# Kernel optimization log

Hardware: AMD Instinct MI355X
Metric: run time of the kernel (lower is better)

## Reference

```python
import jax, jax.numpy as jnp
import numpy as np


def setup_inputs() -> dict:
    key = jax.random.key(0)
    k1, k2, k3, k4 = jax.random.split(key, 4)
    B, C, H, W = 4, 48, 512, 512
    T, ws = 3, 64
    # factor matrices (per TensorMultiplication_einsum, T summation terms)
    # init scale: 1/(init_temperature**(1/3) * sqrt(out_dim)) with init_temperature=1.0
    Ws = jax.random.normal(k2, (T, ws, ws), jnp.float32) / np.sqrt(ws)
    Hs = jax.random.normal(k3, (T, ws, ws), jnp.float32) / np.sqrt(ws)
    Cs = jax.random.normal(k4, (T, C, C), jnp.float32) / np.sqrt(C)
    x = jax.random.normal(k1, (B, C, H, W), jnp.float32)
    return {"x": x, "Ws": Ws, "Hs": Hs, "Cs": Cs, "window_size": ws}


def reference(x, Ws, Hs, Cs, window_size):
    """FeatureProcessingBlock forward:
      window_partition -> sum_t einsum('bchw,wW,hH,cC->bCHW') -> window_reverse.
    The window partition/reverse reshapes are fused into one einsum over the
    blocked view (p,q index the window grid; h,w index within-window pixels).
    """
    B, C, H, W = x.shape
    ws = window_size
    # (B, C, H//ws, ws, W//ws, ws)
    xb = x.reshape(B, C, H // ws, ws, W // ws, ws)
    # sum over T terms and contract w, h, c axes with their factor matrices
    out = jnp.einsum('bcphqw,twW,thH,tcC->bCpHqW', xb, Ws, Hs, Cs)
    return out.reshape(B, C, H, W)
```

## Files before the change

### kernel.cpp

```cpp
#include <hip/hip_runtime.h>
#include <hip/hip_bf16.h>


typedef __attribute__((ext_vector_type(8))) short short8;
typedef __attribute__((ext_vector_type(4))) short short4v;
typedef __attribute__((ext_vector_type(4))) float float4v;

#define SMEM_BYTES 112144

static __device__ __forceinline__ unsigned short f2bf(float f) {
  return __builtin_bit_cast(unsigned short, __float2bfloat16(f));
}
static __device__ __forceinline__ unsigned long long pk4(float a, float b, float c, float d) {
  unsigned long long lo = (unsigned int)((unsigned int)f2bf(a) | ((unsigned int)f2bf(b) << 16));
  unsigned long long hi = (unsigned int)((unsigned int)f2bf(c) | ((unsigned int)f2bf(d) << 16));
  return lo | (hi << 32);
}
static __device__ __forceinline__ void wg_barrier_lds() {
  asm volatile("s_waitcnt lgkmcnt(0)" ::: "memory");
  __builtin_amdgcn_s_barrier();
  asm volatile("" ::: "memory");
}

__global__ __launch_bounds__(512, 2)
void fpb11(const float* __restrict__ x, const float* __restrict__ Ws,
           const float* __restrict__ Hsm, const float* __restrict__ Cs,
           float* __restrict__ out) {
  extern __shared__ char smem[];
  char* Y1F = smem;
  char* Zb  = smem + 49152;
  char* Cf  = smem + 98304;
  char* z16 = smem + 112128;

  int wid = (blockIdx.x & 7) * 128 + (blockIdx.x >> 3);
  int window = wid >> 2, tile = wid & 3;
  int b = window >> 6, p = (window >> 3) & 7, q = window & 7;
  int j0 = tile * 16;

  int tid = threadIdx.x, lane = tid & 63, wave = tid >> 6;
  int lq = lane >> 4, lc = lane & 15;
  int mt = wave & 3, cp = wave >> 2;

  if (tid < 4) ((unsigned int*)z16)[tid] = 0;

  for (int idx = wave; idx < 18; idx += 8) {
    int ss = idx / 3, m = idx - 3 * ss;
    if (lq < 3) {
      short8 v;
      #pragma unroll
      for (int e = 0; e < 8; ++e)
        v[e] = (short)f2bf(Cs[lq * 2304 + (8 * ss + e) * 48 + 16 * m + lc]);
      *(short8*)(Cf + (idx * 16 + lc) * 48 + lq * 16) = v;
    }
  }

  short8 wsf[3][2], hsf[3][2];
  #pragma unroll
  for (int t = 0; t < 3; ++t)
    #pragma unroll
    for (int sv = 0; sv < 2; ++sv) {
      short8 aa, bb;
      #pragma unroll
      for (int e = 0; e < 8; ++e) {
        int k = 32 * sv + 8 * lq + e;
        aa[e] = (short)f2bf(Ws [t * 4096 + k * 64 + j0 + lc]);
        bb[e] = (short)f2bf(Hsm[t * 4096 + k * 64 + 16 * mt + lc]);
      }
      wsf[t][sv] = aa; hsf[t][sv] = bb;
    }

  float4v acc[3][8];
  #pragma unroll
  for (int m = 0; m < 3; ++m)
    #pragma unroll
    for (int i = 0; i < 8; ++i) acc[m][i] = float4v{0.f, 0.f, 0.f, 0.f};

  const float* xbase = x + (((size_t)b * 48) * 512 + p * 64) * 512 + q * 64
                         + (size_t)wave * 262144 + (size_t)lc * 512 + 8 * lq;

  float4v fin[2][8];
  #pragma unroll
  for (int h = 0; h < 2; ++h) {
    const float* src = xbase + (size_t)(32 * h) * 512;
    #pragma unroll
    for (int j2 = 0; j2 < 2; ++j2) {
      const float* r = src + (size_t)(16 * j2) * 512;
      fin[h][4*j2+0] = *(const float4v*)(r);
      fin[h][4*j2+1] = *(const float4v*)(r + 4);
      fin[h][4*j2+2] = *(const float4v*)(r + 32);
      fin[h][4*j2+3] = *(const float4v*)(r + 36);
    }
  }

  for (int s = 0; s < 6; ++s) {
    #pragma unroll
    for (int h = 0; h < 2; ++h) {
      short8 af[4];
      #pragma unroll
      for (int j2 = 0; j2 < 2; ++j2) {
        short8 a0, a1;
        #pragma unroll
        for (int e2 = 0; e2 < 4; ++e2) {
          a0[e2]   = (short)f2bf(fin[h][4*j2+0][e2]);
          a0[4+e2] = (short)f2bf(fin[h][4*j2+1][e2]);
          a1[e2]   = (short)f2bf(fin[h][4*j2+2][e2]);
          a1[4+e2] = (short)f2bf(fin[h][4*j2+3][e2]);
        }
        af[2*j2] = a0; af[2*j2+1] = a1;
      }
      if (s < 5) {
        const float* src = xbase + (size_t)(s + 1) * 2097152 + (size_t)(32 * h) * 512;
        #pragma unroll
        for (int j2 = 0; j2 < 2; ++j2) {
          const float* r = src + (size_t)(16 * j2) * 512;
          fin[h][4*j2+0] = *(const float4v*)(r);
          fin[h][4*j2+1] = *(const float4v*)(r + 4);
          fin[h][4*j2+2] = *(const float4v*)(r + 32);
          fin[h][4*j2+3] = *(const float4v*)(r + 36);
        }
      }
      #pragma unroll
      for (int j2 = 0; j2 < 2; ++j2) {
        int mA  = 2 * h + j2;
        int sv  = mA >> 1;
        int lqp = (2 * mA + (lq >> 1)) & 3;
        int eo  = (lq & 1) * 8;
        #pragma unroll
        for (int t = 0; t < 3; ++t) {
          float4v d = {0.f, 0.f, 0.f, 0.f};
          d = __builtin_amdgcn_mfma_f32_16x16x32_bf16(af[2*j2],   wsf[t][0], d, 0, 0, 0);
          d = __builtin_amdgcn_mfma_f32_16x16x32_bf16(af[2*j2+1], wsf[t][1], d, 0, 0, 0);
          short4v pv;
          pv[0] = (short)f2bf(d[0]); pv[1] = (short)f2bf(d[1]);
          pv[2] = (short)f2bf(d[2]); pv[3] = (short)f2bf(d[3]);
          *(short4v*)(Y1F + ((t * 8 + wave) * 2 + sv) * 1024
                          + (lqp * 16 + lc) * 16 + eo) = pv;
        }
      }
    }
    wg_barrier_lds();

    #pragma unroll
    for (int t = 0; t < 3; ++t) {
      float4v dB[4];
      #pragma unroll
      for (int cj = 0; cj < 4; ++cj) {
        const char* yb = Y1F + ((t * 8 + 4 * cp + cj) * 2) * 1024 + lane * 16;
        short8 y0 = *(const short8*)yb;
        short8 y1 = *(const short8*)(yb + 1024);
        float4v dd = {0.f, 0.f, 0.f, 0.f};
        dd = __builtin_amdgcn_mfma_f32_16x16x32_bf16(hsf[t][0], y0, dd, 0, 0, 0);
        dd = __builtin_amdgcn_mfma_f32_16x16x32_bf16(hsf[t][1], y1, dd, 0, 0, 0);
        dB[cj] = dd;
      }
      #pragma unroll
      for (int r = 0; r < 4; ++r) {
        int px = (16 * mt + 4 * lq + r) * 16 + lc;
        *(unsigned long long*)(Zb + px * 48 + 16 * t + 8 * cp) =
            pk4(dB[0][r], dB[1][r], dB[2][r], dB[3][r]);
      }
    }
    wg_barrier_lds();

    {
      short8 cf[3];
      #pragma unroll
      for (int m = 0; m < 3; ++m) {
        const char* csrc = (lq < 3) ? (Cf + ((s * 3 + m) * 16 + lc) * 48 + lq * 16) : z16;
        cf[m] = *(const short8*)csrc;
      }
      #pragma unroll
      for (int i = 0; i < 8; ++i) {
        int px = 16 * (wave + 8 * i) + lc;
        const char* zsrc = (lq < 3) ? (Zb + px * 48 + 16 * lq) : z16;
        short8 zf = *(const short8*)zsrc;
        acc[0][i] = __builtin_amdgcn_mfma_f32_16x16x32_bf16(cf[0], zf, acc[0][i], 0, 0, 0);
        acc[1][i] = __builtin_amdgcn_mfma_f32_16x16x32_bf16(cf[1], zf, acc[1][i], 0, 0, 0);
        acc[2][i] = __builtin_amdgcn_mfma_f32_16x16x32_bf16(cf[2], zf, acc[2][i], 0, 0, 0);
      }
    }
  }

  #pragma unroll
  for (int m = 0; m < 3; ++m)
    #pragma unroll
    for (int i = 0; i < 8; ++i) {
      int n = wave + 8 * i;
      size_t rowbase = (((size_t)(b * 48 + 16 * m + 4 * lq)) * 512 + p * 64 + n) * 512
                       + q * 64 + j0 + lc;
      #pragma unroll
      for (int r = 0; r < 4; ++r)
        out[rowbase + (size_t)r * 262144] = acc[m][i][r];
    }
}

extern "C" void kernel_launch(void* const* d_in, const int* in_sizes, int n_in,
                              void* d_out, int out_size, void* d_ws, size_t ws_size,
                              hipStream_t stream) {
  (void)in_sizes; (void)n_in; (void)d_ws; (void)ws_size; (void)out_size;
  const float* x   = (const float*)d_in[0];
  const float* Ws  = (const float*)d_in[1];
  const float* Hsm = (const float*)d_in[2];
  const float* Cs  = (const float*)d_in[3];
  float* out = (float*)d_out;
  (void)hipFuncSetAttribute((const void*)fpb11,
                            hipFuncAttributeMaxDynamicSharedMemorySize, SMEM_BYTES);
  fpb11<<<dim3(1024), dim3(512), SMEM_BYTES, stream>>>(x, Ws, Hsm, Cs, out);
}
```

Measured before the change: 155.7 us.

## Software-pipeline the three contraction stages with double-buffered LDS staging

Splits each channel step into two half-steps over channel groups, so there are 12 stages instead of 6. The W-contraction for the next half-step, the H-contraction for the current one and the C-contraction for the previous step now run in the same barrier interval. Y1F and Zb get double buffers, and Zb moves to a per-term planar layout with a 16-byte pixel stride. The goal is to overlap the stages and cut the number of barrier-separated phases. The cost is about 160 KB of LDS, which is near the CU limit, plus some extra prologue and epilogue work.

```diff
diff --git a/kernel.cpp b/kernel.cpp
--- a/kernel.cpp
+++ b/kernel.cpp
@@ -6,15 +6,13 @@
 typedef __attribute__((ext_vector_type(4))) short short4v;
 typedef __attribute__((ext_vector_type(4))) float float4v;
 
-#define SMEM_BYTES 112144
+#define SMEM_BYTES 161296
 
 static __device__ __forceinline__ unsigned short f2bf(float f) {
   return __builtin_bit_cast(unsigned short, __float2bfloat16(f));
 }
-static __device__ __forceinline__ unsigned long long pk4(float a, float b, float c, float d) {
-  unsigned long long lo = (unsigned int)((unsigned int)f2bf(a) | ((unsigned int)f2bf(b) << 16));
-  unsigned long long hi = (unsigned int)((unsigned int)f2bf(c) | ((unsigned int)f2bf(d) << 16));
-  return lo | (hi << 32);
+static __device__ __forceinline__ unsigned int pk2(float a, float b) {
+  return (unsigned int)f2bf(a) | ((unsigned int)f2bf(b) << 16);
 }
 static __device__ __forceinline__ void wg_barrier_lds() {
   asm volatile("s_waitcnt lgkmcnt(0)" ::: "memory");
@@ -23,14 +21,14 @@
 }
 
 __global__ __launch_bounds__(512, 2)
-void fpb11(const float* __restrict__ x, const float* __restrict__ Ws,
+void fpb13(const float* __restrict__ x, const float* __restrict__ Ws,
            const float* __restrict__ Hsm, const float* __restrict__ Cs,
            float* __restrict__ out) {
   extern __shared__ char smem[];
   char* Y1F = smem;
   char* Zb  = smem + 49152;
-  char* Cf  = smem + 98304;
-  char* z16 = smem + 112128;
+  char* Cf  = smem + 147456;
+  char* z16 = smem + 161280;
 
   int wid = (blockIdx.x & 7) * 128 + (blockIdx.x >> 3);
   int window = wid >> 2, tile = wid & 3;
@@ -39,7 +37,8 @@
 
   int tid = threadIdx.x, lane = tid & 63, wave = tid >> 6;
   int lq = lane >> 4, lc = lane & 15;
-  int mt = wave & 3, cp = wave >> 2;
+  int clA = wave & 3, hh = wave >> 2;
+  int mt  = wave & 3, cp = wave >> 2;
 
   if (tid < 4) ((unsigned int*)z16)[tid] = 0;
 
@@ -75,109 +74,130 @@
     #pragma unroll
     for (int i = 0; i < 8; ++i) acc[m][i] = float4v{0.f, 0.f, 0.f, 0.f};
 
-  const float* xbase = x + (((size_t)b * 48) * 512 + p * 64) * 512 + q * 64
-                         + (size_t)wave * 262144 + (size_t)lc * 512 + 8 * lq;
-
-  float4v fin[2][8];
-  #pragma unroll
-  for (int h = 0; h < 2; ++h) {
-    const float* src = xbase + (size_t)(32 * h) * 512;
-    #pragma unroll
-    for (int j2 = 0; j2 < 2; ++j2) {
-      const float* r = src + (size_t)(16 * j2) * 512;
-      fin[h][4*j2+0] = *(const float4v*)(r);
-      fin[h][4*j2+1] = *(const float4v*)(r + 4);
-      fin[h][4*j2+2] = *(const float4v*)(r + 32);
-      fin[h][4*j2+3] = *(const float4v*)(r + 36);
-    }
-  }
-
-  for (int s = 0; s < 6; ++s) {
-    #pragma unroll
-    for (int h = 0; h < 2; ++h) {
-      short8 af[4];
-      #pragma unroll
-      for (int j2 = 0; j2 < 2; ++j2) {
-        short8 a0, a1;
+  const float* xA = x + (((size_t)b * 48) * 512 + p * 64) * 512 + q * 64
+                      + (size_t)clA * 262144 + (size_t)(32 * hh + lc) * 512 + 8 * lq;
+
+  float4v fin[8];
+  #define LOADFIN(vv) do {                                        \
+    const float* srcb_ = xA + (size_t)(vv) * 1048576;             \
+    _Pragma("unroll")                                             \
+    for (int j2_ = 0; j2_ < 2; ++j2_) {                           \
+      const float* r_ = srcb_ + (size_t)j2_ * 8192;               \
+      fin[4*j2_+0] = *(const float4v*)(r_);                       \
+      fin[4*j2_+1] = *(const float4v*)(r_ + 4);                   \
+      fin[4*j2_+2] = *(const float4v*)(r_ + 32);                  \
+      fin[4*j2_+3] = *(const float4v*)(r_ + 36);                  \
+    }                                                             \
+  } while (0)
+
+  #define ABLOCK(vv) do {                                                     \
+    char* yb_ = Y1F + ((vv) & 1) * 24576;                                     \
+    short8 af_[4];                                                            \
+    _Pragma("unroll")                                                         \
+    for (int j2_ = 0; j2_ < 2; ++j2_) {                                       \
+      short8 a0_, a1_;                                                        \
+      _Pragma("unroll")                                                       \
+      for (int e2_ = 0; e2_ < 4; ++e2_) {                                     \
+        a0_[e2_]   = (short)f2bf(fin[4*j2_+0][e2_]);                          \
+        a0_[4+e2_] = (short)f2bf(fin[4*j2_+1][e2_]);                          \
+        a1_[e2_]   = (short)f2bf(fin[4*j2_+2][e2_]);                          \
+        a1_[4+e2_] = (short)f2bf(fin[4*j2_+3][e2_]);                          \
+      }                                                                       \
+      af_[2*j2_] = a0_; af_[2*j2_+1] = a1_;                                   \
+    }                                                                         \
+    if ((vv) < 11) LOADFIN((vv) + 1);                                         \
+    _Pragma("unroll")                                                         \
+    for (int j2_ = 0; j2_ < 2; ++j2_) {                                       \
+      int mA_  = 2 * hh + j2_;                                                \
+      int sv_  = mA_ >> 1;                                                    \
+      int lqp_ = (2 * mA_ + (lq >> 1)) & 3;                                   \
+      int eo_  = (lq & 1) * 8;                                                \
+      _Pragma("unroll")                                                       \
+      for (int t_ = 0; t_ < 3; ++t_) {                                        \
+        float4v d_ = {0.f, 0.f, 0.f, 0.f};                                    \
+        d_ = __builtin_amdgcn_mfma_f32_16x16x32_bf16(af_[2*j2_],   wsf[t_][0], d_, 0, 0, 0); \
+        d_ = __builtin_amdgcn_mfma_f32_16x16x32_bf16(af_[2*j2_+1], wsf[t_][1], d_, 0, 0, 0); \
+        short4v pv_;                                                          \
+        pv_[0] = (short)f2bf(d_[0]); pv_[1] = (short)f2bf(d_[1]);             \
+        pv_[2] = (short)f2bf(d_[2]); pv_[3] = (short)f2bf(d_[3]);             \
+        *(short4v*)(yb_ + ((t_ * 4 + clA) * 2 + sv_) * 1024                   \
+                        + (lqp_ * 16 + lc) * 16 + eo_) = pv_;                 \
+      }                                                                       \
+    }                                                                         \
+  } while (0)
+
+  LOADFIN(0);
+  wg_barrier_lds();
+  ABLOCK(0);
+  wg_barrier_lds();
+
+  #pragma unroll 1
+  for (int v = 0; v < 12; ++v) {
+    {
+      const char* yb = Y1F + (v & 1) * 24576;
+      char* zb = Zb + ((v >> 1) & 1) * 49152;
+      int half = (v & 1) * 8;
+      #pragma unroll
+      for (int t = 0; t < 3; ++t) {
+        float4v dB[2];
         #pragma unroll
-        for (int e2 = 0; e2 < 4; ++e2) {
-          a0[e2]   = (short)f2bf(fin[h][4*j2+0][e2]);
-          a0[4+e2] = (short)f2bf(fin[h][4*j2+1][e2]);
-          a1[e2]   = (short)f2bf(fin[h][4*j2+2][e2]);
-          a1[4+e2] = (short)f2bf(fin[h][4*j2+3][e2]);
+        for (int cj = 0; cj < 2; ++cj) {
+          int cl = 2 * cp + cj;
+          const char* ybs = yb + ((t * 4 + cl) * 2) * 1024 + lane * 16;
+          short8 y0 = *(const short8*)ybs;
+          short8 y1 = *(const short8*)(ybs + 1024);
+          float4v dd = {0.f, 0.f, 0.f, 0.f};
+          dd = __builtin_amdgcn_mfma_f32_16x16x32_bf16(hsf[t][0], y0, dd, 0, 0, 0);
+          dd = __builtin_amdgcn_mfma_f32_16x16x32_bf16(hsf[t][1], y1, dd, 0, 0, 0);
+          dB[cj] = dd;
         }
-        af[2*j2] = a0; af[2*j2+1] = a1;
-      }
-      if (s < 5) {
-        const float* src = xbase + (size_t)(s + 1) * 2097152 + (size_t)(32 * h) * 512;
         #pragma unroll
-        for (int j2 = 0; j2 < 2; ++j2) {
-          const float* r = src + (size_t)(16 * j2) * 512;
-          fin[h][4*j2+0] = *(const float4v*)(r);
-          fin[h][4*j2+1] = *(const float4v*)(r + 4);
-          fin[h][4*j2+2] = *(const float4v*)(r + 32);
-          fin[h][4*j2+3] = *(const float4v*)(r + 36);
+        for (int r = 0; r < 4; ++r) {
+          int px = (16 * mt + 4 * lq + r) * 16 + lc;
+          *(unsigned int*)(zb + t * 16384 + px * 16 + half + 4 * cp) =
+              pk2(dB[0][r], dB[1][r]);
         }
       }
-      #pragma unroll
-      for (int j2 = 0; j2 < 2; ++j2) {
-        int mA  = 2 * h + j2;
-        int sv  = mA >> 1;
-        int lqp = (2 * mA + (lq >> 1)) & 3;
-        int eo  = (lq & 1) * 8;
-        #pragma unroll
-        for (int t = 0; t < 3; ++t) {
-          float4v d = {0.f, 0.f, 0.f, 0.f};
-          d = __builtin_amdgcn_mfma_f32_16x16x32_bf16(af[2*j2],   wsf[t][0], d, 0, 0, 0);
-          d = __builtin_amdgcn_mfma_f32_16x16x32_bf16(af[2*j2+1], wsf[t][1], d, 0, 0, 0);
-          short4v pv;
-          pv[0] = (short)f2bf(d[0]); pv[1] = (short)f2bf(d[1]);
-          pv[2] = (short)f2bf(d[2]); pv[3] = (short)f2bf(d[3]);
-          *(short4v*)(Y1F + ((t * 8 + wave) * 2 + sv) * 1024
-                          + (lqp * 16 + lc) * 16 + eo) = pv;
-        }
-      }
-    }
-    wg_barrier_lds();
-
-    #pragma unroll
-    for (int t = 0; t < 3; ++t) {
-      float4v dB[4];
-      #pragma unroll
-      for (int cj = 0; cj < 4; ++cj) {
-        const char* yb = Y1F + ((t * 8 + 4 * cp + cj) * 2) * 1024 + lane * 16;
-        short8 y0 = *(const short8*)yb;
-        short8 y1 = *(const short8*)(yb + 1024);
-        float4v dd = {0.f, 0.f, 0.f, 0.f};
-        dd = __builtin_amdgcn_mfma_f32_16x16x32_bf16(hsf[t][0], y0, dd, 0, 0, 0);
-        dd = __builtin_amdgcn_mfma_f32_16x16x32_bf16(hsf[t][1], y1, dd, 0, 0, 0);
-        dB[cj] = dd;
-      }
-      #pragma unroll
-      for (int r = 0; r < 4; ++r) {
-        int px = (16 * mt + 4 * lq + r) * 16 + lc;
-        *(unsigned long long*)(Zb + px * 48 + 16 * t + 8 * cp) =
-            pk4(dB[0][r], dB[1][r], dB[2][r], dB[3][r]);
-      }
-    }
-    wg_barrier_lds();
-
-    {
+    }
+    if (v < 11) ABLOCK(v + 1);
+    if ((v & 1) && v >= 3) {
+      int Sp = (v >> 1) - 1;
+      const char* zb = Zb + (Sp & 1) * 49152;
       short8 cf[3];
       #pragma unroll
       for (int m = 0; m < 3; ++m) {
-        const char* csrc = (lq < 3) ? (Cf + ((s * 3 + m) * 16 + lc) * 48 + lq * 16) : z16;
+        const char* csrc = (lq < 3) ? (Cf + ((Sp * 3 + m) * 16 + lc) * 48 + lq * 16) : z16;
         cf[m] = *(const short8*)csrc;
       }
       #pragma unroll
       for (int i = 0; i < 8; ++i) {
         int px = 16 * (wave + 8 * i) + lc;
-        const char* zsrc = (lq < 3) ? (Zb + px * 48 + 16 * lq) : z16;
+        const char* zsrc = (lq < 3) ? (zb + lq * 16384 + px * 16) : z16;
         short8 zf = *(const short8*)zsrc;
         acc[0][i] = __builtin_amdgcn_mfma_f32_16x16x32_bf16(cf[0], zf, acc[0][i], 0, 0, 0);
         acc[1][i] = __builtin_amdgcn_mfma_f32_16x16x32_bf16(cf[1], zf, acc[1][i], 0, 0, 0);
         acc[2][i] = __builtin_amdgcn_mfma_f32_16x16x32_bf16(cf[2], zf, acc[2][i], 0, 0, 0);
       }
+    }
+    wg_barrier_lds();
+  }
+
+  {
+    const char* zb = Zb + 1 * 49152;
+    short8 cf[3];
+    #pragma unroll
+    for (int m = 0; m < 3; ++m) {
+      const char* csrc = (lq < 3) ? (Cf + ((5 * 3 + m) * 16 + lc) * 48 + lq * 16) : z16;
+      cf[m] = *(const short8*)csrc;
+    }
+    #pragma unroll
+    for (int i = 0; i < 8; ++i) {
+      int px = 16 * (wave + 8 * i) + lc;
+      const char* zsrc = (lq < 3) ? (zb + lq * 16384 + px * 16) : z16;
+      short8 zf = *(const short8*)zsrc;
+      acc[0][i] = __builtin_amdgcn_mfma_f32_16x16x32_bf16(cf[0], zf, acc[0][i], 0, 0, 0);
+      acc[1][i] = __builtin_amdgcn_mfma_f32_16x16x32_bf16(cf[1], zf, acc[1][i], 0, 0, 0);
+      acc[2][i] = __builtin_amdgcn_mfma_f32_16x16x32_bf16(cf[2], zf, acc[2][i], 0, 0, 0);
     }
   }
 
@@ -203,7 +223,7 @@
   const float* Hsm = (const float*)d_in[2];
   const float* Cs  = (const float*)d_in[3];
   float* out = (float*)d_out;
-  (void)hipFuncSetAttribute((const void*)fpb11,
+  (void)hipFuncSetAttribute((const void*)fpb13,
                             hipFuncAttributeMaxDynamicSharedMemorySize, SMEM_BYTES);
-  fpb11<<<dim3(1024), dim3(512), SMEM_BYTES, stream>>>(x, Ws, Hsm, Cs, out);
-}
+  fpb13<<<dim3(1024), dim3(512), SMEM_BYTES, stream>>>(x, Ws, Hsm, Cs, out);
+}
```

After: 191.2 us. 22.8% more time.
